# Optimization experiments

Measured on AMD Instinct MI355X. Metric: run time of the kernel, lower is better.

Reference implementation:

```python
import jax, jax.numpy as jnp
import numpy as np

B, W, N, L = 64, 256, 128, 64


def setup_inputs() -> dict:
    key = jax.random.key(0)
    k1, k2, k3 = jax.random.split(key, 3)
    x = jax.random.normal(k1, (B, W, L), dtype=jnp.float32)
    shapelets = jax.random.normal(k2, (N, L), dtype=jnp.float32)
    cls_w = jax.random.normal(k3, (1, N), dtype=jnp.float32) * 0.1
    cls_b = jnp.zeros((1,), dtype=jnp.float32)
    return {"x": x, "shapelets": shapelets, "cls_w": cls_w, "cls_b": cls_b}


def reference(x, shapelets, cls_w, cls_b):
    # diffs: [B, W, N, L] broadcast subtract
    diffs = x[:, :, None, :] - shapelets[None, None, :, :]
    # L2 norm over shapelet-length axis -> [B, W, N]
    discrim = jnp.sqrt(jnp.sum(diffs * diffs, axis=3))
    # min over windows -> [B, N]
    min_discrim = jnp.min(discrim, axis=1)
    # tiny classifier: Linear(N, 1) + sigmoid -> [B, 1]
    logits = min_discrim @ cls_w.T + cls_b
    return jax.nn.sigmoid(logits)
```

## Files before the change

kernel.cpp:

```cpp
#include <hip/hip_runtime.h>
#include <cfloat>
#include <cmath>

constexpr int B = 64;
constexpr int W = 256;
constexpr int N = 128;
constexpr int L = 64;
constexpr int NC = 16;
constexpr int WPB = W / NC;

template <int CTRL>
__device__ __forceinline__ float dpp_add(float v) {
  return v + __int_as_float(__builtin_amdgcn_update_dpp(
                 0, __float_as_int(v), CTRL, 0xF, 0xF, true));
}

__global__ __launch_bounds__(256) void shapelet_min_kernel(
    const float* __restrict__ x, const float* __restrict__ shp,
    float* __restrict__ part) {
  __shared__ float xs[WPB * L];
  __shared__ float xnorm_s[WPB];

  const int b = blockIdx.x >> 4;
  const int c = blockIdx.x & 15;
  const int tid = threadIdx.x;
  const int oct = tid & 7;
  const int grp = tid >> 3;
  const int n0 = grp * 4;

  {
    const float4* xg =
        (const float4*)(x + ((size_t)b * W + (size_t)c * WPB) * L);
    float4 v = xg[tid];
    ((float4*)xs)[tid] = v;
    float p = v.x * v.x + v.y * v.y + v.z * v.z + v.w * v.w;
    p = dpp_add<0xB1>(p);
    p = dpp_add<0x4E>(p);
    p = dpp_add<0x141>(p);
    p = dpp_add<0x140>(p);
    if ((tid & 15) == 0) xnorm_s[tid >> 4] = p;
  }

  const float4* g0 = (const float4*)(shp + (size_t)(n0 + 0) * L + oct * 8);
  const float4* g1 = (const float4*)(shp + (size_t)(n0 + 1) * L + oct * 8);
  const float4* g2 = (const float4*)(shp + (size_t)(n0 + 2) * L + oct * 8);
  const float4* g3 = (const float4*)(shp + (size_t)(n0 + 3) * L + oct * 8);
  const float4 s0a = g0[0], s0b = g0[1];
  const float4 s1a = g1[0], s1b = g1[1];
  const float4 s2a = g2[0], s2b = g2[1];
  const float4 s3a = g3[0], s3b = g3[1];

  __syncthreads();

  float best0 = FLT_MAX, best1 = FLT_MAX, best2 = FLT_MAX, best3 = FLT_MAX;
  for (int w = 0; w < WPB; ++w) {
    const float4* xr = (const float4*)(xs + (size_t)w * L + oct * 8);
    const float4 xa = xr[0];
    const float4 xb = xr[1];

    float d0 = xa.x * s0a.x + xa.y * s0a.y;
    float d1 = xa.x * s1a.x + xa.y * s1a.y;
    float d2 = xa.x * s2a.x + xa.y * s2a.y;
    float d3 = xa.x * s3a.x + xa.y * s3a.y;
    d0 = fmaf(xa.z, s0a.z, d0); d0 = fmaf(xa.w, s0a.w, d0);
    d1 = fmaf(xa.z, s1a.z, d1); d1 = fmaf(xa.w, s1a.w, d1);
    d2 = fmaf(xa.z, s2a.z, d2); d2 = fmaf(xa.w, s2a.w, d2);
    d3 = fmaf(xa.z, s3a.z, d3); d3 = fmaf(xa.w, s3a.w, d3);
    d0 = fmaf(xb.x, s0b.x, d0); d0 = fmaf(xb.y, s0b.y, d0);
    d1 = fmaf(xb.x, s1b.x, d1); d1 = fmaf(xb.y, s1b.y, d1);
    d2 = fmaf(xb.x, s2b.x, d2); d2 = fmaf(xb.y, s2b.y, d2);
    d3 = fmaf(xb.x, s3b.x, d3); d3 = fmaf(xb.y, s3b.y, d3);
    d0 = fmaf(xb.z, s0b.z, d0); d0 = fmaf(xb.w, s0b.w, d0);
    d1 = fmaf(xb.z, s1b.z, d1); d1 = fmaf(xb.w, s1b.w, d1);
    d2 = fmaf(xb.z, s2b.z, d2); d2 = fmaf(xb.w, s2b.w, d2);
    d3 = fmaf(xb.z, s3b.z, d3); d3 = fmaf(xb.w, s3b.w, d3);

    d0 = dpp_add<0xB1>(d0);  d1 = dpp_add<0xB1>(d1);
    d2 = dpp_add<0xB1>(d2);  d3 = dpp_add<0xB1>(d3);
    d0 = dpp_add<0x4E>(d0);  d1 = dpp_add<0x4E>(d1);
    d2 = dpp_add<0x4E>(d2);  d3 = dpp_add<0x4E>(d3);
    d0 = dpp_add<0x141>(d0); d1 = dpp_add<0x141>(d1);
    d2 = dpp_add<0x141>(d2); d3 = dpp_add<0x141>(d3);

    const float xn = xnorm_s[w];
    best0 = fminf(best0, fmaf(-2.f, d0, xn));
    best1 = fminf(best1, fmaf(-2.f, d1, xn));
    best2 = fminf(best2, fmaf(-2.f, d2, xn));
    best3 = fminf(best3, fmaf(-2.f, d3, xn));
  }

  if (oct == 0) {
    float4 o;
    o.x = best0; o.y = best1; o.z = best2; o.w = best3;
    *(float4*)(part + ((size_t)b * NC + c) * N + n0) = o;
  }
}

__global__ __launch_bounds__(128) void shapelet_head_kernel(
    const float* __restrict__ part, const float* __restrict__ shp,
    const float* __restrict__ cls_w, const float* __restrict__ cls_b,
    float* __restrict__ out) {
  const int b = blockIdx.x;
  const int n = threadIdx.x;

  float m = FLT_MAX;
#pragma unroll
  for (int c = 0; c < NC; ++c)
    m = fminf(m, part[((size_t)b * NC + c) * N + n]);

  float sn = 0.f;
  {
    const float4* sg = (const float4*)(shp + (size_t)n * L);
#pragma unroll
    for (int i = 0; i < L / 4; ++i) {
      float4 v = sg[i];
      sn = fmaf(v.x, v.x, sn);
      sn = fmaf(v.y, v.y, sn);
      sn = fmaf(v.z, v.z, sn);
      sn = fmaf(v.w, v.w, sn);
    }
  }

  float d2 = fmaxf(m + sn, 0.f);
  float v = sqrtf(d2) * cls_w[n];

#pragma unroll
  for (int off = 32; off > 0; off >>= 1) v += __shfl_down(v, off, 64);

  __shared__ float red[2];
  if ((n & 63) == 0) red[n >> 6] = v;
  __syncthreads();
  if (n == 0) {
    float z = red[0] + red[1] + cls_b[0];
    out[b] = 1.0f / (1.0f + expf(-z));
  }
}

extern "C" void kernel_launch(void* const* d_in, const int* in_sizes, int n_in,
                              void* d_out, int out_size, void* d_ws,
                              size_t ws_size, hipStream_t stream) {
  const float* x = (const float*)d_in[0];
  const float* shp = (const float*)d_in[1];
  const float* cls_w = (const float*)d_in[2];
  const float* cls_b = (const float*)d_in[3];
  float* out = (float*)d_out;
  float* part = (float*)d_ws;

  shapelet_min_kernel<<<B * NC, 256, 0, stream>>>(x, shp, part);
  shapelet_head_kernel<<<B, 128, 0, stream>>>(part, shp, cls_w, cls_b, out);
}
```

Before: 68.80 us.

## Fuse head into min kernel via last-block atomic counter per batch

Merges the two kernels into one. Each block bumps a per-batch global atomic counter, and the last block to finish for a batch reduces the partial minima and computes the sigmoid output. The shapelet squared norms are now computed in the main kernel from registers already loaded and added into the partials, so the head no longer re-reads the shapelets. This removes one kernel launch and its gap. In exchange it adds a threadfence, an atomic and an extra barrier to every block, and it relies on the counter resetting correctly between calls.

```diff
diff --git a/kernel.cpp b/kernel.cpp
--- a/kernel.cpp
+++ b/kernel.cpp
@@ -9,17 +9,26 @@
 constexpr int NC = 16;
 constexpr int WPB = W / NC;
 
+__device__ int g_cnt[B];
+
 template <int CTRL>
 __device__ __forceinline__ float dpp_add(float v) {
   return v + __int_as_float(__builtin_amdgcn_update_dpp(
                  0, __float_as_int(v), CTRL, 0xF, 0xF, true));
 }
 
-__global__ __launch_bounds__(256) void shapelet_min_kernel(
-    const float* __restrict__ x, const float* __restrict__ shp,
-    float* __restrict__ part) {
+__global__ __launch_bounds__(256)
+__attribute__((amdgpu_waves_per_eu(4, 4)))
+void shapelet_fused_kernel(const float* __restrict__ x,
+                           const float* __restrict__ shp,
+                           const float* __restrict__ cls_w,
+                           const float* __restrict__ cls_b,
+                           float* __restrict__ part,
+                           float* __restrict__ out) {
   __shared__ float xs[WPB * L];
   __shared__ float xnorm_s[WPB];
+  __shared__ int s_last;
+  __shared__ float red[4];
 
   const int b = blockIdx.x >> 4;
   const int c = blockIdx.x & 15;
@@ -49,6 +58,29 @@
   const float4 s1a = g1[0], s1b = g1[1];
   const float4 s2a = g2[0], s2b = g2[1];
   const float4 s3a = g3[0], s3b = g3[1];
+
+  float q0 = s0a.x * s0a.x + s0a.y * s0a.y;
+  float q1 = s1a.x * s1a.x + s1a.y * s1a.y;
+  float q2 = s2a.x * s2a.x + s2a.y * s2a.y;
+  float q3 = s3a.x * s3a.x + s3a.y * s3a.y;
+  q0 = fmaf(s0a.z, s0a.z, q0); q0 = fmaf(s0a.w, s0a.w, q0);
+  q1 = fmaf(s1a.z, s1a.z, q1); q1 = fmaf(s1a.w, s1a.w, q1);
+  q2 = fmaf(s2a.z, s2a.z, q2); q2 = fmaf(s2a.w, s2a.w, q2);
+  q3 = fmaf(s3a.z, s3a.z, q3); q3 = fmaf(s3a.w, s3a.w, q3);
+  q0 = fmaf(s0b.x, s0b.x, q0); q0 = fmaf(s0b.y, s0b.y, q0);
+  q1 = fmaf(s1b.x, s1b.x, q1); q1 = fmaf(s1b.y, s1b.y, q1);
+  q2 = fmaf(s2b.x, s2b.x, q2); q2 = fmaf(s2b.y, s2b.y, q2);
+  q3 = fmaf(s3b.x, s3b.x, q3); q3 = fmaf(s3b.y, s3b.y, q3);
+  q0 = fmaf(s0b.z, s0b.z, q0); q0 = fmaf(s0b.w, s0b.w, q0);
+  q1 = fmaf(s1b.z, s1b.z, q1); q1 = fmaf(s1b.w, s1b.w, q1);
+  q2 = fmaf(s2b.z, s2b.z, q2); q2 = fmaf(s2b.w, s2b.w, q2);
+  q3 = fmaf(s3b.z, s3b.z, q3); q3 = fmaf(s3b.w, s3b.w, q3);
+  q0 = dpp_add<0xB1>(q0);  q1 = dpp_add<0xB1>(q1);
+  q2 = dpp_add<0xB1>(q2);  q3 = dpp_add<0xB1>(q3);
+  q0 = dpp_add<0x4E>(q0);  q1 = dpp_add<0x4E>(q1);
+  q2 = dpp_add<0x4E>(q2);  q3 = dpp_add<0x4E>(q3);
+  q0 = dpp_add<0x141>(q0); q1 = dpp_add<0x141>(q1);
+  q2 = dpp_add<0x141>(q2); q3 = dpp_add<0x141>(q3);
 
   __syncthreads();
 
@@ -91,47 +123,36 @@
 
   if (oct == 0) {
     float4 o;
-    o.x = best0; o.y = best1; o.z = best2; o.w = best3;
+    o.x = best0 + q0; o.y = best1 + q1; o.z = best2 + q2; o.w = best3 + q3;
     *(float4*)(part + ((size_t)b * NC + c) * N + n0) = o;
   }
-}
 
-__global__ __launch_bounds__(128) void shapelet_head_kernel(
-    const float* __restrict__ part, const float* __restrict__ shp,
-    const float* __restrict__ cls_w, const float* __restrict__ cls_b,
-    float* __restrict__ out) {
-  const int b = blockIdx.x;
-  const int n = threadIdx.x;
+  __syncthreads();
+  if (tid == 0) {
+    __threadfence();
+    int done = atomicAdd(&g_cnt[b], 1);
+    s_last = (done == NC - 1) ? 1 : 0;
+    if (done == NC - 1) atomicExch(&g_cnt[b], 0);
+  }
+  __syncthreads();
+  if (!s_last) return;
 
-  float m = FLT_MAX;
+  __threadfence();
+  float v = 0.f;
+  if (tid < N) {
+    const float* pb = part + (size_t)b * NC * N + tid;
+    float m = FLT_MAX;
 #pragma unroll
-  for (int c = 0; c < NC; ++c)
-    m = fminf(m, part[((size_t)b * NC + c) * N + n]);
-
-  float sn = 0.f;
-  {
-    const float4* sg = (const float4*)(shp + (size_t)n * L);
-#pragma unroll
-    for (int i = 0; i < L / 4; ++i) {
-      float4 v = sg[i];
-      sn = fmaf(v.x, v.x, sn);
-      sn = fmaf(v.y, v.y, sn);
-      sn = fmaf(v.z, v.z, sn);
-      sn = fmaf(v.w, v.w, sn);
-    }
+    for (int cc = 0; cc < NC; ++cc) m = fminf(m, pb[cc * N]);
+    float d2 = fmaxf(m, 0.f);
+    v = sqrtf(d2) * cls_w[tid];
   }
-
-  float d2 = fmaxf(m + sn, 0.f);
-  float v = sqrtf(d2) * cls_w[n];
-
 #pragma unroll
   for (int off = 32; off > 0; off >>= 1) v += __shfl_down(v, off, 64);
-
-  __shared__ float red[2];
-  if ((n & 63) == 0) red[n >> 6] = v;
+  if ((tid & 63) == 0) red[tid >> 6] = v;
   __syncthreads();
-  if (n == 0) {
-    float z = red[0] + red[1] + cls_b[0];
+  if (tid == 0) {
+    float z = red[0] + red[1] + red[2] + red[3] + cls_b[0];
     out[b] = 1.0f / (1.0f + expf(-z));
   }
 }
@@ -146,6 +167,6 @@
   float* out = (float*)d_out;
   float* part = (float*)d_ws;
 
-  shapelet_min_kernel<<<B * NC, 256, 0, stream>>>(x, shp, part);
-  shapelet_head_kernel<<<B, 128, 0, stream>>>(part, shp, cls_w, cls_b, out);
+  shapelet_fused_kernel<<<B * NC, 256, 0, stream>>>(x, shp, cls_w, cls_b,
+                                                    part, out);
 }
```

Result: slower. 92.82 us (+34.9%).
